# Kernel optimization log

Measured on AMD Instinct MI355X. Metric: run time of the kernel, lower is better.

The kernel has to match this reference:

```python
import jax, jax.numpy as jnp
import numpy as np

HIDDEN = 1024   # hidden_dimensions (dim_in)
NUM_HEADS = 16
HEAD_DIM = 64   # dim_q == dim_k == output_dimensions per head
BATCH = 4
SEQ = 2048


def setup_inputs() -> dict:
    key = jax.random.key(0)
    ks = jax.random.split(key, 11)
    s = 1.0 / np.sqrt(HIDDEN)
    so = 1.0 / np.sqrt(NUM_HEADS * HEAD_DIM)
    return {
        "Q": jax.random.normal(ks[0], (BATCH, SEQ, HIDDEN), jnp.float32),
        "K": jax.random.normal(ks[1], (BATCH, SEQ, HIDDEN), jnp.float32),
        "V": jax.random.normal(ks[2], (BATCH, SEQ, HIDDEN), jnp.float32),
        # per-head projection weights stacked over the head axis
        "Wq": jax.random.uniform(ks[3], (NUM_HEADS, HIDDEN, HEAD_DIM), jnp.float32, -s, s),
        "bq": jax.random.uniform(ks[4], (NUM_HEADS, HEAD_DIM), jnp.float32, -s, s),
        "Wk": jax.random.uniform(ks[5], (NUM_HEADS, HIDDEN, HEAD_DIM), jnp.float32, -s, s),
        "bk": jax.random.uniform(ks[6], (NUM_HEADS, HEAD_DIM), jnp.float32, -s, s),
        "Wv": jax.random.uniform(ks[7], (NUM_HEADS, HIDDEN, HEAD_DIM), jnp.float32, -s, s),
        "bv": jax.random.uniform(ks[8], (NUM_HEADS, HEAD_DIM), jnp.float32, -s, s),
        # output projection: concat(num_heads*head_dim) -> hidden
        "Wo": jax.random.uniform(ks[9], (NUM_HEADS * HEAD_DIM, HIDDEN), jnp.float32, -so, so),
        "bo": jax.random.uniform(ks[10], (HIDDEN,), jnp.float32, -so, so),
    }


def reference(Q, K, V, Wq, bq, Wk, bk, Wv, bv, Wo, bo):
    # Per-head linear projections (batched over heads instead of Python loop)
    q = jnp.einsum("bsd,hdk->bhsk", Q, Wq) + bq[None, :, None, :]  # [B,H,S,dk]
    k = jnp.einsum("bsd,hdk->bhsk", K, Wk) + bk[None, :, None, :]
    v = jnp.einsum("bsd,hdk->bhsk", V, Wv) + bv[None, :, None, :]
    # Scaled dot-product attention
    scale = 1.0 / jnp.sqrt(jnp.asarray(k.shape[-1], q.dtype))
    scores = jnp.einsum("bhqk,bhsk->bhqs", q, k) * scale          # [B,H,S,S]
    attn = jax.nn.softmax(scores, axis=-1)
    o = jnp.einsum("bhqs,bhsk->bhqk", attn, v)                     # [B,H,S,dk]
    # Concatenate heads along the feature dim, then output linear
    B, H, S, dk = o.shape
    concat = jnp.transpose(o, (0, 2, 1, 3)).reshape(B, S, H * dk)  # [B,S,H*dk]
    return concat @ Wo + bo                                        # [B,S,HIDDEN]
```

## Files before the change

kernel.cpp:

```cpp
#include <hip/hip_runtime.h>
#include <hip/hip_bf16.h>
#include <stdint.h>

typedef unsigned short u16;
typedef uint32_t u32;
typedef __attribute__((ext_vector_type(4))) float f32x4;
typedef __attribute__((ext_vector_type(16))) float f32x16;
typedef __attribute__((ext_vector_type(8))) short s8v;
typedef __attribute__((ext_vector_type(4))) unsigned short u16x4;
typedef __attribute__((ext_vector_type(2))) uint32_t u32x2;

#define SCALE_Q 0.18033688f

union PU { s8v v; u32 w[4]; };

__device__ __forceinline__ u16 f2bf(float f) {
  union { float f; uint32_t u; } v; v.f = f;
  uint32_t r = v.u + 0x7fffu + ((v.u >> 16) & 1u);
  return (u16)(r >> 16);
}

__device__ __forceinline__ u32 pk2(float lo, float hi) {
  __hip_bfloat162 h = __float22bfloat162_rn(float2{lo, hi});
  union { __hip_bfloat162 h; u32 u; } c; c.h = h; return c.u;
}

__device__ __forceinline__ void gl16(const void* g, void* l) {
  __builtin_amdgcn_global_load_lds((const __attribute__((address_space(1))) u32*)g,
                                   (__attribute__((address_space(3))) u32*)l, 16, 0, 0);
}

#define BARRIER()  __builtin_amdgcn_s_barrier()
#define SCHEDB()   __builtin_amdgcn_sched_barrier(0)
#define SGB(m, n)  __builtin_amdgcn_sched_group_barrier((m), (n), 0)

__global__ __launch_bounds__(256) void k_conv3(const float* __restrict__ a, const float* __restrict__ b,
                                               const float* __restrict__ c, u16* __restrict__ oa,
                                               u16* __restrict__ ob, u16* __restrict__ oc) {
  int which = blockIdx.y;
  const float* in = which == 0 ? a : (which == 1 ? b : c);
  u16* out = which == 0 ? oa : (which == 1 ? ob : oc);
  int i = (blockIdx.x * 256 + threadIdx.x) * 4;
  float4 v = *(const float4*)(in + i);
  u16x4 o; o[0] = f2bf(v.x); o[1] = f2bf(v.y); o[2] = f2bf(v.z); o[3] = f2bf(v.w);
  *(u16x4*)(out + i) = o;
}

__global__ __launch_bounds__(256) void k_convW_t(const float* __restrict__ wq, const float* __restrict__ wk,
                                                 const float* __restrict__ wv, u16* __restrict__ oq,
                                                 u16* __restrict__ ok, u16* __restrict__ ov) {
  __shared__ float T[64][65];
  const int z = blockIdx.z, h = blockIdx.y, d0 = blockIdx.x * 64;
  const float* w = z == 0 ? wq : (z == 1 ? wk : wv);
  u16* o = z == 0 ? oq : (z == 1 ? ok : ov);
  const float scale = z == 0 ? SCALE_Q : 1.0f;
  const int t = threadIdx.x;
#pragma unroll
  for (int i = 0; i < 16; ++i) {
    int f = t + i * 256;
    T[f >> 6][f & 63] = w[(h * 1024 + d0 + (f >> 6)) * 64 + (f & 63)];
  }
  __syncthreads();
#pragma unroll
  for (int i = 0; i < 16; ++i) {
    int g = t + i * 256;
    o[(h * 64 + (g >> 6)) * 1024 + d0 + (g & 63)] = f2bf(T[g & 63][g >> 6] * scale);
  }
}

__global__ __launch_bounds__(256) void k_convWo_t(const float* __restrict__ w, u16* __restrict__ o) {
  __shared__ float T[64][65];
  const int n0 = blockIdx.x * 64, c0 = blockIdx.y * 64;
  const int t = threadIdx.x;
#pragma unroll
  for (int i = 0; i < 16; ++i) {
    int f = t + i * 256;
    T[f >> 6][f & 63] = w[(c0 + (f >> 6)) * 1024 + n0 + (f & 63)];
  }
  __syncthreads();
#pragma unroll
  for (int i = 0; i < 16; ++i) {
    int g = t + i * 256;
    o[(n0 + (g >> 6)) * 1024 + c0 + (g & 63)] = f2bf(T[g & 63][g >> 6]);
  }
}

__global__ __launch_bounds__(256) void k_gemm3(
    const u16* __restrict__ Aq, const u16* __restrict__ Ak, const u16* __restrict__ Av,
    const u16* __restrict__ Bq, const u16* __restrict__ Bk, const u16* __restrict__ Bv,
    const float* __restrict__ bqp, const float* __restrict__ bkp, const float* __restrict__ bvp,
    u16* __restrict__ oq, u16* __restrict__ ok, u16* __restrict__ ov) {
  constexpr int Kd = 1024, Nd = 1024;
  __shared__ alignas(16) u16 As[2][128 * 64];
  __shared__ alignas(16) u16 Bs[2][128 * 64];
  const int z = blockIdx.z;
  const u16* A = z == 0 ? Aq : (z == 1 ? Ak : Av);
  const u16* Bt = z == 0 ? Bq : (z == 1 ? Bk : Bv);
  const float* bias = z == 0 ? bqp : (z == 1 ? bkp : bvp);

  const int t = threadIdx.x;
  const int lane = t & 63;
  const int w = t >> 6;
  const int wm = w >> 1, wn = w & 1;
  const int lr = lane & 15, lg = lane >> 4;
  const long bm = blockIdx.x * 128, bn = blockIdx.y * 128;
  const int r8 = lane >> 3, c8 = lane & 7;
  const int chunk = c8 ^ r8;

  f32x4 acc[4][4] = {};
  const u16* Ap = A + (bm + w * 8 + r8) * (long)Kd + chunk * 8;
  const u16* Bp = Bt + (bn + w * 8 + r8) * (long)Kd + chunk * 8;

  auto GSTAGE = [&](u16* Asb, u16* Bsb, int kt) {
#pragma unroll
    for (int p = 0; p < 4; ++p) {
      gl16(Ap + (long)p * 32 * Kd + kt, Asb + (p * 32 + w * 8) * 64);
      gl16(Bp + (long)p * 32 * Kd + kt, Bsb + (p * 32 + w * 8) * 64);
    }
  };
  auto GCOMP = [&](const u16* Asb, const u16* Bsb) {
#pragma unroll
    for (int ks = 0; ks < 2; ++ks) {
      s8v af[4], bf[4];
#pragma unroll
      for (int i = 0; i < 4; ++i) {
        int arow = wm * 64 + i * 16 + lr;
        af[i] = *(const s8v*)(Asb + arow * 64 + (((ks * 4 + lg) ^ (arow & 7)) * 8));
        int brow = wn * 64 + i * 16 + lr;
        bf[i] = *(const s8v*)(Bsb + brow * 64 + (((ks * 4 + lg) ^ (brow & 7)) * 8));
      }
#pragma unroll
      for (int i = 0; i < 4; ++i)
#pragma unroll
        for (int j = 0; j < 4; ++j)
          acc[i][j] = __builtin_amdgcn_mfma_f32_16x16x32_bf16(af[i], bf[j], acc[i][j], 0, 0, 0);
    }
  };

  GSTAGE(As[0], Bs[0], 0);
  for (int kt = 0; kt < 16; ++kt) {
    BARRIER();
    SCHEDB();
    if (kt < 15) {
      GSTAGE(As[(kt + 1) & 1], Bs[(kt + 1) & 1], (kt + 1) * 64);
      asm volatile("s_waitcnt vmcnt(8)" ::: "memory");
    } else {
      asm volatile("s_waitcnt vmcnt(0)" ::: "memory");
    }
    SCHEDB();
    BARRIER();
    SCHEDB();
    GCOMP(As[kt & 1], Bs[kt & 1]);
  }

  const float bscale = z == 0 ? SCALE_Q : 1.0f;
  float bcol[4];
#pragma unroll
  for (int j = 0; j < 4; ++j) bcol[j] = bias[bn + wn * 64 + j * 16 + lr] * bscale;

  if (z < 2) {
    u16* C = z == 0 ? oq : ok;
#pragma unroll
    for (int i = 0; i < 4; ++i) {
      long m0 = bm + wm * 64 + i * 16 + lg * 4;
#pragma unroll
      for (int j = 0; j < 4; ++j) {
        long n = bn + wn * 64 + j * 16 + lr;
#pragma unroll
        for (int r = 0; r < 4; ++r)
          C[(m0 + r) * Nd + n] = f2bf(acc[i][j][r] + bcol[j]);
      }
    }
  } else {
    u16* C = ov;
    int lgp = ((lg & 1) << 1) | (lg >> 1);
#pragma unroll
    for (int i = 0; i < 4; ++i) {
      long m0 = bm + wm * 64 + i * 16 + lgp * 4;
      int b = (int)(m0 >> 11), s0 = (int)(m0 & 2047);
#pragma unroll
      for (int j = 0; j < 4; ++j) {
        int n = (int)(bn + wn * 64 + j * 16 + lr);
        int h = n >> 6, dv = n & 63;
        u32x2 cc;
        cc[0] = pk2(acc[i][j][0] + bcol[j], acc[i][j][1] + bcol[j]);
        cc[1] = pk2(acc[i][j][2] + bcol[j], acc[i][j][3] + bcol[j]);
        *(u32x2*)(C + (long)((b * 16 + h) * 64 + dv) * 2048 + s0) = cc;
      }
    }
  }
}

__global__ __launch_bounds__(256) void k_gemmo(const u16* __restrict__ A, const u16* __restrict__ Bt,
                                               const float* __restrict__ bias, float* __restrict__ C) {
  constexpr int Kd = 1024, Nd = 1024;
  __shared__ alignas(16) u16 As[2][128 * 64];
  __shared__ alignas(16) u16 Bs[2][128 * 64];
  const int t = threadIdx.x;
  const int lane = t & 63;
  const int w = t >> 6;
  const int wm = w >> 1, wn = w & 1;
  const int lr = lane & 15, lg = lane >> 4;
  const long bm = blockIdx.x * 128, bn = blockIdx.y * 128;
  const int r8 = lane >> 3, c8 = lane & 7;
  const int chunk = c8 ^ r8;

  f32x4 acc[4][4] = {};
  const u16* Ap = A + (bm + w * 8 + r8) * (long)Kd + chunk * 8;
  const u16* Bp = Bt + (bn + w * 8 + r8) * (long)Kd + chunk * 8;

  auto GSTAGE = [&](u16* Asb, u16* Bsb, int kt) {
#pragma unroll
    for (int p = 0; p < 4; ++p) {
      gl16(Ap + (long)p * 32 * Kd + kt, Asb + (p * 32 + w * 8) * 64);
      gl16(Bp + (long)p * 32 * Kd + kt, Bsb + (p * 32 + w * 8) * 64);
    }
  };
  auto GCOMP = [&](const u16* Asb, const u16* Bsb) {
#pragma unroll
    for (int ks = 0; ks < 2; ++ks) {
      s8v af[4], bf[4];
#pragma unroll
      for (int i = 0; i < 4; ++i) {
        int arow = wm * 64 + i * 16 + lr;
        af[i] = *(const s8v*)(Asb + arow * 64 + (((ks * 4 + lg) ^ (arow & 7)) * 8));
        int brow = wn * 64 + i * 16 + lr;
        bf[i] = *(const s8v*)(Bsb + brow * 64 + (((ks * 4 + lg) ^ (brow & 7)) * 8));
      }
#pragma unroll
      for (int i = 0; i < 4; ++i)
#pragma unroll
        for (int j = 0; j < 4; ++j)
          acc[i][j] = __builtin_amdgcn_mfma_f32_16x16x32_bf16(af[i], bf[j], acc[i][j], 0, 0, 0);
    }
  };

  GSTAGE(As[0], Bs[0], 0);
  for (int kt = 0; kt < 16; ++kt) {
    BARRIER();
    SCHEDB();
    if (kt < 15) {
      GSTAGE(As[(kt + 1) & 1], Bs[(kt + 1) & 1], (kt + 1) * 64);
      asm volatile("s_waitcnt vmcnt(8)" ::: "memory");
    } else {
      asm volatile("s_waitcnt vmcnt(0)" ::: "memory");
    }
    SCHEDB();
    BARRIER();
    SCHEDB();
    GCOMP(As[kt & 1], Bs[kt & 1]);
  }

  float bcol[4];
#pragma unroll
  for (int j = 0; j < 4; ++j) bcol[j] = bias[bn + wn * 64 + j * 16 + lr];
#pragma unroll
  for (int i = 0; i < 4; ++i) {
    long m0 = bm + wm * 64 + i * 16 + lg * 4;
#pragma unroll
    for (int j = 0; j < 4; ++j) {
      long n = bn + wn * 64 + j * 16 + lr;
#pragma unroll
      for (int r = 0; r < 4; ++r)
        C[(m0 + r) * Nd + n] = acc[i][j][r] + bcol[j];
    }
  }
}

__global__ __launch_bounds__(256, 2) void k_attn(const u16* __restrict__ q, const u16* __restrict__ k,
                                                 const u16* __restrict__ vT, u16* __restrict__ o) {
  __shared__ alignas(16) u16 Ks[4][64 * 64];
  __shared__ alignas(16) u16 Vs[4][64 * 64];
  const int t = threadIdx.x;
  const int lane = t & 63;
  const int wv = t >> 6;
  const int l5 = lane & 31, hi = lane >> 5;
  const int r8 = lane >> 3, c8 = lane & 7;
  const int rx = l5 & 7;

  const int wg = blockIdx.x;
  const int ob = (wg & 7) * 64 + (wg >> 3);
  const int qt = ob & 7, h = (ob >> 3) & 15, b = ob >> 7;

  const int qrow0 = qt * 256 + wv * 64 + l5;
  const u16* qpA = q + ((long)(b * 2048 + qrow0) * 1024 + h * 64);
  const u16* qpB = qpA + 32 * 1024;
  s8v qfA[4], qfB[4];
#pragma unroll
  for (int s = 0; s < 4; ++s) {
    qfA[s] = *(const s8v*)(qpA + s * 16 + hi * 8);
    qfB[s] = *(const s8v*)(qpB + s * 16 + hi * 8);
  }

  const u16* Kpp = k + (long)b * 2048 * 1024 + h * 64 + (long)r8 * 1024 + ((c8 ^ r8) * 8);
  const u16* Vpp = vT + (long)(b * 16 + h) * 131072 + (long)r8 * 2048 + ((c8 ^ r8) * 8);

  f32x16 accA0 = {}, accA1 = {}, accB0 = {}, accB1 = {};
  float lA = 0.f, lB = 0.f;

  int offs[4];
#pragma unroll
  for (int s = 0; s < 4; ++s) offs[s] = ((2 * s + hi) ^ rx) * 8;
  const int rb0 = l5 * 64, rb1 = rb0 + 2048;

  auto ASTAGE = [&](int buf, int kv) {
#pragma unroll
    for (int r0 = 0; r0 < 2; ++r0) {
      int rowo = wv * 16 + r0 * 8;
      gl16(Kpp + ((long)kv + rowo) * 1024, &Ks[buf][rowo * 64]);
      gl16(Vpp + (long)rowo * 2048 + kv,   &Vs[buf][rowo * 64]);
    }
  };

  auto EXPPACK = [&](const f32x16& sv, PU& u0, PU& u1, float& l) {
#pragma unroll
    for (int r1 = 0; r1 < 4; ++r1) {
      float p0 = __builtin_amdgcn_exp2f(sv[4 * r1 + 0]);
      float p1 = __builtin_amdgcn_exp2f(sv[4 * r1 + 1]);
      float p2 = __builtin_amdgcn_exp2f(sv[4 * r1 + 2]);
      float p3 = __builtin_amdgcn_exp2f(sv[4 * r1 + 3]);
      l += (p0 + p1) + (p2 + p3);
      if (r1 < 2) {
        u0.w[(r1 & 1) * 2 + 0] = pk2(p0, p1);
        u0.w[(r1 & 1) * 2 + 1] = pk2(p2, p3);
      } else {
        u1.w[(r1 & 1) * 2 + 0] = pk2(p0, p1);
        u1.w[(r1 & 1) * 2 + 1] = pk2(p2, p3);
      }
    }
  };

  auto ATILE = [&](int buf) {
    const u16* Ksb = Ks[buf];
    const u16* Vsb = Vs[buf];
    PU paU[4], pbU[4];
    f32x16 sA0 = {}, sB0 = {}, sA1 = {}, sB1 = {};
    s8v kf0[4], kf1[4];
#pragma unroll
    for (int s = 0; s < 4; ++s) {
      kf0[s] = *(const s8v*)(Ksb + rb0 + offs[s]);
      kf1[s] = *(const s8v*)(Ksb + rb1 + offs[s]);
    }
#pragma unroll
    for (int s = 0; s < 4; ++s) {
      sA0 = __builtin_amdgcn_mfma_f32_32x32x16_bf16(kf0[s], qfA[s], sA0, 0, 0, 0);
      sB0 = __builtin_amdgcn_mfma_f32_32x32x16_bf16(kf0[s], qfB[s], sB0, 0, 0, 0);
    }
#pragma unroll
    for (int g = 0; g < 4; ++g) { SGB(0x100, 2); SGB(0x8, 2); }
    SCHEDB();
#pragma unroll
    for (int s = 0; s < 4; ++s) {
      sA1 = __builtin_amdgcn_mfma_f32_32x32x16_bf16(kf1[s], qfA[s], sA1, 0, 0, 0);
      sB1 = __builtin_amdgcn_mfma_f32_32x32x16_bf16(kf1[s], qfB[s], sB1, 0, 0, 0);
    }
    EXPPACK(sA0, paU[0], paU[1], lA);
    EXPPACK(sB0, pbU[0], pbU[1], lB);
#pragma unroll
    for (int g = 0; g < 8; ++g) { SGB(0x8, 1); SGB(0x2, 9); }
    SCHEDB();
    s8v vf0[4], vf1[4];
#pragma unroll
    for (int s = 0; s < 4; ++s) {
      vf0[s] = *(const s8v*)(Vsb + rb0 + offs[s]);
      vf1[s] = *(const s8v*)(Vsb + rb1 + offs[s]);
    }
#pragma unroll
    for (int s2 = 0; s2 < 2; ++s2) {
      accA0 = __builtin_amdgcn_mfma_f32_32x32x16_bf16(vf0[s2], paU[s2].v, accA0, 0, 0, 0);
      accA1 = __builtin_amdgcn_mfma_f32_32x32x16_bf16(vf1[s2], paU[s2].v, accA1, 0, 0, 0);
      accB0 = __builtin_amdgcn_mfma_f32_32x32x16_bf16(vf0[s2], pbU[s2].v, accB0, 0, 0, 0);
      accB1 = __builtin_amdgcn_mfma_f32_32x32x16_bf16(vf1[s2], pbU[s2].v, accB1, 0, 0, 0);
    }
    EXPPACK(sA1, paU[2], paU[3], lA);
    EXPPACK(sB1, pbU[2], pbU[3], lB);
#pragma unroll
    for (int g = 0; g < 8; ++g) { SGB(0x100, 1); SGB(0x8, 1); SGB(0x2, 9); }
    SCHEDB();
#pragma unroll
    for (int s2 = 2; s2 < 4; ++s2) {
      accA0 = __builtin_amdgcn_mfma_f32_32x32x16_bf16(vf0[s2], paU[s2].v, accA0, 0, 0, 0);
      accA1 = __builtin_amdgcn_mfma_f32_32x32x16_bf16(vf1[s2], paU[s2].v, accA1, 0, 0, 0);
      accB0 = __builtin_amdgcn_mfma_f32_32x32x16_bf16(vf0[s2], pbU[s2].v, accB0, 0, 0, 0);
      accB1 = __builtin_amdgcn_mfma_f32_32x32x16_bf16(vf1[s2], pbU[s2].v, accB1, 0, 0, 0);
    }
  };

  ASTAGE(0, 0);
  ASTAGE(1, 64);
  asm volatile("s_waitcnt vmcnt(4)" ::: "memory");
  SCHEDB();
  BARRIER();
  SCHEDB();
  for (int tt = 0; tt < 30; ++tt) {
    ASTAGE((tt + 2) & 3, (tt + 2) * 64);
    ATILE(tt & 3);
    asm volatile("s_waitcnt vmcnt(4) lgkmcnt(0)" ::: "memory");
    SCHEDB();
    BARRIER();
    SCHEDB();
  }
  ATILE(30 & 3);
  asm volatile("s_waitcnt vmcnt(0) lgkmcnt(0)" ::: "memory");
  SCHEDB();
  BARRIER();
  SCHEDB();
  ATILE(31 & 3);

  lA += __shfl_xor(lA, 32);
  lB += __shfl_xor(lB, 32);
  float iA = 1.0f / lA, iB = 1.0f / lB;
  u16* opA = o + ((long)(b * 2048 + qrow0) * 1024 + h * 64);
  u16* opB = opA + 32 * 1024;
#pragma unroll
  for (int kb = 0; kb < 2; ++kb) {
#pragma unroll
    for (int r1 = 0; r1 < 4; ++r1) {
      u32x2 ca, cb;
      float a0 = kb ? accA1[4 * r1 + 0] : accA0[4 * r1 + 0];
      float a1 = kb ? accA1[4 * r1 + 1] : accA0[4 * r1 + 1];
      float a2 = kb ? accA1[4 * r1 + 2] : accA0[4 * r1 + 2];
      float a3 = kb ? accA1[4 * r1 + 3] : accA0[4 * r1 + 3];
      ca[0] = pk2(a0 * iA, a1 * iA);
      ca[1] = pk2(a2 * iA, a3 * iA);
      *(u32x2*)(opA + kb * 32 + r1 * 8 + hi * 4) = ca;
      float b0 = kb ? accB1[4 * r1 + 0] : accB0[4 * r1 + 0];
      float b1 = kb ? accB1[4 * r1 + 1] : accB0[4 * r1 + 1];
      float b2 = kb ? accB1[4 * r1 + 2] : accB0[4 * r1 + 2];
      float b3 = kb ? accB1[4 * r1 + 3] : accB0[4 * r1 + 3];
      cb[0] = pk2(b0 * iB, b1 * iB);
      cb[1] = pk2(b2 * iB, b3 * iB);
      *(u32x2*)(opB + kb * 32 + r1 * 8 + hi * 4) = cb;
    }
  }
}

extern "C" void kernel_launch(void* const* d_in, const int* in_sizes, int n_in,
                              void* d_out, int out_size, void* d_ws, size_t ws_size,
                              hipStream_t stream) {
  const float* Q  = (const float*)d_in[0];
  const float* K  = (const float*)d_in[1];
  const float* V  = (const float*)d_in[2];
  const float* Wq = (const float*)d_in[3];
  const float* bq = (const float*)d_in[4];
  const float* Wk = (const float*)d_in[5];
  const float* bk = (const float*)d_in[6];
  const float* Wv = (const float*)d_in[7];
  const float* bvp = (const float*)d_in[8];
  const float* Wo = (const float*)d_in[9];
  const float* bo = (const float*)d_in[10];
  float* out = (float*)d_out;

  char* ws = (char*)d_ws;
  const size_t MB16 = (size_t)8192 * 1024 * 2;
  u16* Qb  = (u16*)(ws);
  u16* Kb  = (u16*)(ws + MB16);
  u16* Vb  = (u16*)(ws + 2 * MB16);
  u16* WqT = (u16*)(ws + 3 * MB16);
  u16* WkT = (u16*)(ws + 3 * MB16 + ((size_t)2 << 20));
  u16* WvT = (u16*)(ws + 3 * MB16 + ((size_t)4 << 20));
  u16* WoT = (u16*)(ws + 3 * MB16 + ((size_t)6 << 20));
  u16* qws = (u16*)(ws + 3 * MB16 + ((size_t)8 << 20));
  u16* kws = (u16*)(ws + 4 * MB16 + ((size_t)8 << 20));
  u16* vTs = (u16*)(ws + 5 * MB16 + ((size_t)8 << 20));
  u16* ows = Qb;

  k_conv3<<<dim3(8192, 3), 256, 0, stream>>>(Q, K, V, Qb, Kb, Vb);
  k_convW_t<<<dim3(16, 16, 3), 256, 0, stream>>>(Wq, Wk, Wv, WqT, WkT, WvT);
  k_convWo_t<<<dim3(16, 16), 256, 0, stream>>>(Wo, WoT);

  k_gemm3<<<dim3(64, 8, 3), 256, 0, stream>>>(Qb, Kb, Vb, WqT, WkT, WvT,
                                              bq, bk, bvp, qws, kws, vTs);

  k_attn<<<dim3(512), 256, 0, stream>>>(qws, kws, vTs, ows);

  k_gemmo<<<dim3(64, 8), 256, 0, stream>>>(ows, WoT, bo, out);
}
```

Before: 200.8 us.

## Fuse fp32-to-bf16 input conversion into the QKV projection GEMM

Removes the separate conversion kernel for Q/K/V activations. The projection GEMM now reads fp32 activations directly into registers, converts them to bf16 and writes them swizzled into LDS, while weights still arrive via direct global-to-LDS loads. LDS drops from double to single buffering, with register prefetch of the next A tile. This saves a full fp32 read plus bf16 write and read of three 32MB-class tensors, but doubles the A-side global traffic inside the GEMM and loses LDS double buffering.

```diff
diff --git a/kernel.cpp b/kernel.cpp
--- a/kernel.cpp
+++ b/kernel.cpp
@@ -9,6 +9,7 @@
 typedef __attribute__((ext_vector_type(8))) short s8v;
 typedef __attribute__((ext_vector_type(4))) unsigned short u16x4;
 typedef __attribute__((ext_vector_type(2))) uint32_t u32x2;
+typedef __attribute__((ext_vector_type(4))) uint32_t u32x4;
 
 #define SCALE_Q 0.18033688f
 
@@ -33,18 +34,7 @@
 #define BARRIER()  __builtin_amdgcn_s_barrier()
 #define SCHEDB()   __builtin_amdgcn_sched_barrier(0)
 #define SGB(m, n)  __builtin_amdgcn_sched_group_barrier((m), (n), 0)
-
-__global__ __launch_bounds__(256) void k_conv3(const float* __restrict__ a, const float* __restrict__ b,
-                                               const float* __restrict__ c, u16* __restrict__ oa,
-                                               u16* __restrict__ ob, u16* __restrict__ oc) {
-  int which = blockIdx.y;
-  const float* in = which == 0 ? a : (which == 1 ? b : c);
-  u16* out = which == 0 ? oa : (which == 1 ? ob : oc);
-  int i = (blockIdx.x * 256 + threadIdx.x) * 4;
-  float4 v = *(const float4*)(in + i);
-  u16x4 o; o[0] = f2bf(v.x); o[1] = f2bf(v.y); o[2] = f2bf(v.z); o[3] = f2bf(v.w);
-  *(u16x4*)(out + i) = o;
-}
+#define MEMPIN()   asm volatile("" ::: "memory")
 
 __global__ __launch_bounds__(256) void k_convW_t(const float* __restrict__ wq, const float* __restrict__ wk,
                                                  const float* __restrict__ wv, u16* __restrict__ oq,
@@ -85,16 +75,16 @@
   }
 }
 
-__global__ __launch_bounds__(256) void k_gemm3(
-    const u16* __restrict__ Aq, const u16* __restrict__ Ak, const u16* __restrict__ Av,
+__global__ __launch_bounds__(256) void k_gemm3f(
+    const float* __restrict__ Aq, const float* __restrict__ Ak, const float* __restrict__ Av,
     const u16* __restrict__ Bq, const u16* __restrict__ Bk, const u16* __restrict__ Bv,
     const float* __restrict__ bqp, const float* __restrict__ bkp, const float* __restrict__ bvp,
     u16* __restrict__ oq, u16* __restrict__ ok, u16* __restrict__ ov) {
   constexpr int Kd = 1024, Nd = 1024;
-  __shared__ alignas(16) u16 As[2][128 * 64];
-  __shared__ alignas(16) u16 Bs[2][128 * 64];
+  __shared__ alignas(16) u16 As[128 * 64];
+  __shared__ alignas(16) u16 Bs[128 * 64];
   const int z = blockIdx.z;
-  const u16* A = z == 0 ? Aq : (z == 1 ? Ak : Av);
+  const float* A = z == 0 ? Aq : (z == 1 ? Ak : Av);
   const u16* Bt = z == 0 ? Bq : (z == 1 ? Bk : Bv);
   const float* bias = z == 0 ? bqp : (z == 1 ? bkp : bvp);
 
@@ -107,27 +97,47 @@
   const int r8 = lane >> 3, c8 = lane & 7;
   const int chunk = c8 ^ r8;
 
+  const int arow_s = t >> 3, achk = t & 7;
+  const int aswz = (achk ^ (arow_s & 7)) * 8;
+  const float* Apf = A + (bm + arow_s) * (long)Kd + achk * 8;
+  const u16* Bp = Bt + (bn + w * 8 + r8) * (long)Kd + chunk * 8;
+
   f32x4 acc[4][4] = {};
-  const u16* Ap = A + (bm + w * 8 + r8) * (long)Kd + chunk * 8;
-  const u16* Bp = Bt + (bn + w * 8 + r8) * (long)Kd + chunk * 8;
-
-  auto GSTAGE = [&](u16* Asb, u16* Bsb, int kt) {
-#pragma unroll
-    for (int p = 0; p < 4; ++p) {
-      gl16(Ap + (long)p * 32 * Kd + kt, Asb + (p * 32 + w * 8) * 64);
-      gl16(Bp + (long)p * 32 * Kd + kt, Bsb + (p * 32 + w * 8) * 64);
-    }
-  };
-  auto GCOMP = [&](const u16* Asb, const u16* Bsb) {
+  float4 fa[4][2];
+
+  auto ALOAD = [&](int kt) {
+#pragma unroll
+    for (int j = 0; j < 4; ++j) {
+      fa[j][0] = *(const float4*)(Apf + (long)j * 32 * Kd + kt);
+      fa[j][1] = *(const float4*)(Apf + (long)j * 32 * Kd + kt + 4);
+    }
+  };
+  auto AWRITE = [&]() {
+#pragma unroll
+    for (int j = 0; j < 4; ++j) {
+      u32x4 pk;
+      pk[0] = pk2(fa[j][0].x, fa[j][0].y);
+      pk[1] = pk2(fa[j][0].z, fa[j][0].w);
+      pk[2] = pk2(fa[j][1].x, fa[j][1].y);
+      pk[3] = pk2(fa[j][1].z, fa[j][1].w);
+      *(u32x4*)(&As[(j * 32 + arow_s) * 64 + aswz]) = pk;
+    }
+  };
+  auto BSTG = [&](int kt) {
+#pragma unroll
+    for (int p = 0; p < 4; ++p)
+      gl16(Bp + (long)p * 32 * Kd + kt, Bs + (p * 32 + w * 8) * 64);
+  };
+  auto GCOMP = [&]() {
 #pragma unroll
     for (int ks = 0; ks < 2; ++ks) {
       s8v af[4], bf[4];
 #pragma unroll
       for (int i = 0; i < 4; ++i) {
         int arow = wm * 64 + i * 16 + lr;
-        af[i] = *(const s8v*)(Asb + arow * 64 + (((ks * 4 + lg) ^ (arow & 7)) * 8));
+        af[i] = *(const s8v*)(&As[arow * 64 + (((ks * 4 + lg) ^ (arow & 7)) * 8)]);
         int brow = wn * 64 + i * 16 + lr;
-        bf[i] = *(const s8v*)(Bsb + brow * 64 + (((ks * 4 + lg) ^ (brow & 7)) * 8));
+        bf[i] = *(const s8v*)(&Bs[brow * 64 + (((ks * 4 + lg) ^ (brow & 7)) * 8)]);
       }
 #pragma unroll
       for (int i = 0; i < 4; ++i)
@@ -137,20 +147,25 @@
     }
   };
 
-  GSTAGE(As[0], Bs[0], 0);
+  ALOAD(0);
   for (int kt = 0; kt < 16; ++kt) {
     BARRIER();
     SCHEDB();
+    AWRITE();
+    MEMPIN();
+    BSTG(kt * 64);
+    MEMPIN();
     if (kt < 15) {
-      GSTAGE(As[(kt + 1) & 1], Bs[(kt + 1) & 1], (kt + 1) * 64);
-      asm volatile("s_waitcnt vmcnt(8)" ::: "memory");
+      ALOAD((kt + 1) * 64);
+      MEMPIN();
+      asm volatile("s_waitcnt vmcnt(8) lgkmcnt(0)" ::: "memory");
     } else {
-      asm volatile("s_waitcnt vmcnt(0)" ::: "memory");
+      asm volatile("s_waitcnt vmcnt(0) lgkmcnt(0)" ::: "memory");
     }
     SCHEDB();
     BARRIER();
     SCHEDB();
-    GCOMP(As[kt & 1], Bs[kt & 1]);
+    GCOMP();
   }
 
   const float bscale = z == 0 ? SCALE_Q : 1.0f;
@@ -424,12 +439,12 @@
       ca[0] = pk2(a0 * iA, a1 * iA);
       ca[1] = pk2(a2 * iA, a3 * iA);
       *(u32x2*)(opA + kb * 32 + r1 * 8 + hi * 4) = ca;
-      float b0 = kb ? accB1[4 * r1 + 0] : accB0[4 * r1 + 0];
-      float b1 = kb ? accB1[4 * r1 + 1] : accB0[4 * r1 + 1];
-      float b2 = kb ? accB1[4 * r1 + 2] : accB0[4 * r1 + 2];
-      float b3 = kb ? accB1[4 * r1 + 3] : accB0[4 * r1 + 3];
-      cb[0] = pk2(b0 * iB, b1 * iB);
-      cb[1] = pk2(b2 * iB, b3 * iB);
+      float b0v = kb ? accB1[4 * r1 + 0] : accB0[4 * r1 + 0];
+      float b1v = kb ? accB1[4 * r1 + 1] : accB0[4 * r1 + 1];
+      float b2v = kb ? accB1[4 * r1 + 2] : accB0[4 * r1 + 2];
+      float b3v = kb ? accB1[4 * r1 + 3] : accB0[4 * r1 + 3];
+      cb[0] = pk2(b0v * iB, b1v * iB);
+      cb[1] = pk2(b2v * iB, b3v * iB);
       *(u32x2*)(opB + kb * 32 + r1 * 8 + hi * 4) = cb;
     }
   }
@@ -453,24 +468,20 @@
 
   char* ws = (char*)d_ws;
   const size_t MB16 = (size_t)8192 * 1024 * 2;
-  u16* Qb  = (u16*)(ws);
-  u16* Kb  = (u16*)(ws + MB16);
-  u16* Vb  = (u16*)(ws + 2 * MB16);
-  u16* WqT = (u16*)(ws + 3 * MB16);
-  u16* WkT = (u16*)(ws + 3 * MB16 + ((size_t)2 << 20));
-  u16* WvT = (u16*)(ws + 3 * MB16 + ((size_t)4 << 20));
-  u16* WoT = (u16*)(ws + 3 * MB16 + ((size_t)6 << 20));
-  u16* qws = (u16*)(ws + 3 * MB16 + ((size_t)8 << 20));
-  u16* kws = (u16*)(ws + 4 * MB16 + ((size_t)8 << 20));
-  u16* vTs = (u16*)(ws + 5 * MB16 + ((size_t)8 << 20));
-  u16* ows = Qb;
-
-  k_conv3<<<dim3(8192, 3), 256, 0, stream>>>(Q, K, V, Qb, Kb, Vb);
+  u16* WqT = (u16*)(ws);
+  u16* WkT = (u16*)(ws + ((size_t)2 << 20));
+  u16* WvT = (u16*)(ws + ((size_t)4 << 20));
+  u16* WoT = (u16*)(ws + ((size_t)6 << 20));
+  u16* qws = (u16*)(ws + ((size_t)8 << 20));
+  u16* kws = (u16*)(ws + ((size_t)8 << 20) + MB16);
+  u16* vTs = (u16*)(ws + ((size_t)8 << 20) + 2 * MB16);
+  u16* ows = (u16*)(ws + ((size_t)8 << 20) + 3 * MB16);
+
   k_convW_t<<<dim3(16, 16, 3), 256, 0, stream>>>(Wq, Wk, Wv, WqT, WkT, WvT);
   k_convWo_t<<<dim3(16, 16), 256, 0, stream>>>(Wo, WoT);
 
-  k_gemm3<<<dim3(64, 8, 3), 256, 0, stream>>>(Qb, Kb, Vb, WqT, WkT, WvT,
-                                              bq, bk, bvp, qws, kws, vTs);
+  k_gemm3f<<<dim3(64, 8, 3), 256, 0, stream>>>(Q, K, V, WqT, WkT, WvT,
+                                               bq, bk, bvp, qws, kws, vTs);
 
   k_attn<<<dim3(512), 256, 0, stream>>>(qws, kws, vTs, ows);
 
```

Result: faster. 186.2 us (median of 2 runs) (-7.3%).
